# Kernel tuning notes

Measured on AMD Instinct MI355X. Metric: run time of the kernel, lower is better.

## Reference

```python
import jax, jax.numpy as jnp
import numpy as np

W_BITS = 8
A_BITS = 8


def sym_quant(x, num_bits):
    # Symmetric per-last-dim abs-max quantization (SymQuantizer.forward, ndim<=3,
    # layerwise=False): s = (2^(b-1)-1)/(max|x| + 1e-6); q = round(x*s)/(s+1e-6)
    max_abs = jnp.max(jnp.abs(x), axis=-1, keepdims=True)
    s = (2.0 ** (num_bits - 1) - 1.0) / (max_abs + 1e-6)
    return jnp.round(x * s) / (s + 1e-6)


def setup_inputs() -> dict:
    key = jax.random.key(0)
    kx, kw = jax.random.split(key)
    B, S, NX, NF = 4, 2048, 1600, 6400
    x = jax.random.normal(kx, (B, S, NX), dtype=jnp.float32)
    weight = 0.02 * jax.random.normal(kw, (NX, NF), dtype=jnp.float32)  # Conv1D: [nx, nf]
    bias = jnp.zeros((NF,), dtype=jnp.float32)
    return {"x": x, "weight": weight, "bias": bias}


def reference(x, weight, bias):
    # quantize weights per-row (over nf), quantize activations per-token (over nx)
    wq = sym_quant(weight, W_BITS)
    xq = sym_quant(x, A_BITS)
    # addmm(bias, x.view(-1, nx), weight) then reshape back
    return jnp.einsum("bsx,xf->bsf", xq, wq) + bias
```

## Files before the change

kernel.cpp:

```cpp
#include <hip/hip_runtime.h>
#include <stdint.h>

typedef _Float16 f16;
typedef _Float16 f16x4 __attribute__((ext_vector_type(4)));
typedef _Float16 f16x8 __attribute__((ext_vector_type(8)));
typedef float f32x4 __attribute__((ext_vector_type(4)));

#define K_DIM 1600
#define NF_DIM 6400
#define KPAD 1664
#define NKT 26
#define KPB (KPAD * 2)

#define ABYTES 32768
#define BBYTES 40960
#define BUFSZ (ABYTES + BBYTES)
#define BOFF ABYTES

__device__ __forceinline__ void async_copy16(const void* g, void* l) {
    __builtin_amdgcn_global_load_lds(
        (const __attribute__((address_space(1))) void*)(uintptr_t)g,
        (__attribute__((address_space(3))) void*)(uint32_t)(uintptr_t)l,
        16, 0, 0);
}

__device__ __forceinline__ float blockMax(float v, float* sm) {
#pragma unroll
    for (int off = 32; off > 0; off >>= 1)
        v = fmaxf(v, __shfl_down(v, off, 64));
    int wid = threadIdx.x >> 6, lane = threadIdx.x & 63;
    if (lane == 0) sm[wid] = v;
    __syncthreads();
    if (threadIdx.x == 0) {
        float m = sm[0];
        for (int i = 1; i < (int)(blockDim.x >> 6); ++i) m = fmaxf(m, sm[i]);
        sm[0] = m;
    }
    __syncthreads();
    return sm[0];
}

__global__ void quant_x_kernel(const float* __restrict__ x, f16* __restrict__ qx,
                               float* __restrict__ ax) {
    __shared__ float sm[4];
    size_t row = blockIdx.x;
    const float* xr = x + row * (size_t)K_DIM;
    float m = 0.f;
    const int n4 = K_DIM >> 2;
    for (int i = threadIdx.x; i < n4; i += blockDim.x) {
        float4 v = ((const float4*)xr)[i];
        m = fmaxf(fmaxf(fmaxf(fabsf(v.x), fabsf(v.y)), fmaxf(fabsf(v.z), fabsf(v.w))), m);
    }
    m = blockMax(m, sm);
    float s = 127.0f / (m + 1e-6f);
    if (threadIdx.x == 0) ax[row] = 1.0f / (s + 1e-6f);
    f16* qr = qx + row * (size_t)KPAD;
    for (int i = threadIdx.x; i < n4; i += blockDim.x) {
        float4 v = ((const float4*)xr)[i];
        f16x4 q;
        q[0] = (f16)rintf(v.x * s);
        q[1] = (f16)rintf(v.y * s);
        q[2] = (f16)rintf(v.z * s);
        q[3] = (f16)rintf(v.w * s);
        *(f16x4*)&qr[i * 4] = q;
    }
    if (threadIdx.x < 16) {
        f16x4 z = {};
        *(f16x4*)&qr[K_DIM + threadIdx.x * 4] = z;
    }
}

__global__ void wscale_kernel(const float* __restrict__ w, float* __restrict__ sw) {
    __shared__ float sm[4];
    size_t k = blockIdx.x;
    const float* wr = w + k * (size_t)NF_DIM;
    float m = 0.f;
    const int n4 = NF_DIM >> 2;
    for (int i = threadIdx.x; i < n4; i += blockDim.x) {
        float4 v = ((const float4*)wr)[i];
        m = fmaxf(fmaxf(fmaxf(fabsf(v.x), fabsf(v.y)), fmaxf(fabsf(v.z), fabsf(v.w))), m);
    }
    m = blockMax(m, sm);
    if (threadIdx.x == 0) sw[k] = 127.0f / (m + 1e-6f);
}

__global__ void wtq_kernel(const float* __restrict__ w, const float* __restrict__ sw,
                           f16* __restrict__ wqt) {
    __shared__ f16 t[64][80];
    int k0 = blockIdx.x * 64;
    int f0 = blockIdx.y * 64;
    int tid = threadIdx.x;
    if (k0 >= K_DIM) {
        int fr = tid >> 2;
        int ch = (tid & 3) << 4;
        float4 z = {};
        float4* dst = (float4*)&wqt[(size_t)(f0 + fr) * KPAD + k0 + ch];
        dst[0] = z;
        dst[1] = z;
        return;
    }
    int rr = tid >> 4;
    int cc = (tid & 15) << 2;
#pragma unroll
    for (int i = 0; i < 4; ++i) {
        int r = rr + i * 16;
        float s = sw[k0 + r];
        float inv = 1.0f / (s + 1e-6f);
        float4 v = *(const float4*)&w[(size_t)(k0 + r) * NF_DIM + f0 + cc];
        t[cc + 0][r] = (f16)(rintf(v.x * s) * inv);
        t[cc + 1][r] = (f16)(rintf(v.y * s) * inv);
        t[cc + 2][r] = (f16)(rintf(v.z * s) * inv);
        t[cc + 3][r] = (f16)(rintf(v.w * s) * inv);
    }
    __syncthreads();
    int fr = tid >> 2;
    int ch = (tid & 3) << 4;
    const float4* src = (const float4*)&t[fr][ch];
    float4* dst = (float4*)&wqt[(size_t)(f0 + fr) * KPAD + k0 + ch];
    dst[0] = src[0];
    dst[1] = src[1];
}

__global__ __launch_bounds__(512, 1) void gemm256x320(
    const f16* __restrict__ A,
    const f16* __restrict__ Bt,
    const float* __restrict__ ax,
    const float* __restrict__ bias,
    float* __restrict__ C, int M, int N) {
    extern __shared__ char lds[];

    const int tid = threadIdx.x;
    const int lane = tid & 63;
    const int wv = tid >> 6;
    const int wm = wv >> 2;
    const int wn = wv & 3;
    const int lr = lane & 15;
    const int lg = lane >> 4;

    const int bid = blockIdx.x;
    const int cpx = gridDim.x >> 3;
    const int swz = (bid & 7) * cpx + (bid >> 3);
    const int tm = swz & 31;
    const int tn = swz >> 5;
    const size_t m0 = (size_t)tm * 256, n0 = (size_t)tn * 320;

    const int srow8 = lane >> 3;
    const int sslot = (lane & 7) ^ srow8;
    const char* pA = (const char*)A + (m0 + (size_t)(wv * 32 + srow8)) * KPB + sslot * 16;
    const char* pB = (const char*)Bt + (n0 + (size_t)(wv * 40 + srow8)) * KPB + sslot * 16;
    const int LA0 = wv * 4096 + lane * 16;
    const int LB0 = BOFF + wv * 5120 + lane * 16;

#define ST_A(bufo, t)                                                          \
    {                                                                          \
        const char* g_ = pA + (size_t)(t) * 128;                               \
        _Pragma("unroll") for (int j_ = 0; j_ < 4; ++j_)                       \
            async_copy16(g_ + (size_t)(j_ * 8) * KPB,                          \
                         lds + (bufo) + LA0 + j_ * 1024);                      \
    }
#define ST_B(bufo, t)                                                          \
    {                                                                          \
        const char* g_ = pB + (size_t)(t) * 128;                               \
        _Pragma("unroll") for (int c_ = 0; c_ < 5; ++c_)                       \
            async_copy16(g_ + (size_t)(c_ * 8) * KPB,                          \
                         lds + (bufo) + LB0 + c_ * 1024);                      \
    }

    const int adr0 = (wm * 128 + lr) * 128 + ((((lg)) ^ (lr & 7)) << 4);
    const int adr1 = (wm * 128 + lr) * 128 + (((4 + lg) ^ (lr & 7)) << 4);
    const int bdr0 = BOFF + (wn * 80 + lr) * 128 + (((lg) ^ (lr & 7)) << 4);
    const int bdr1 = BOFF + (wn * 80 + lr) * 128 + (((4 + lg) ^ (lr & 7)) << 4);

#define RD_P(dst, bufo, p, AOFF)                                       \
    {                                                                  \
        const char* p_ = lds + (bufo) + (AOFF) + (p) * 4096;           \
        dst[0] = *(const f16x8*)(p_);                                  \
        dst[1] = *(const f16x8*)(p_ + 2048);                           \
    }
#define RD_B5(dst, bufo, BOFFK)                                        \
    {                                                                  \
        const char* p_ = lds + (bufo) + (BOFFK);                       \
        _Pragma("unroll") for (int n_ = 0; n_ < 5; ++n_)               \
            dst[n_] = *(const f16x8*)(p_ + n_ * 2048);                 \
    }
#define RD_B01(dst, bufo, BOFFK)                                       \
    {                                                                  \
        const char* p_ = lds + (bufo) + (BOFFK);                       \
        dst[0] = *(const f16x8*)(p_);                                  \
        dst[1] = *(const f16x8*)(p_ + 2048);                           \
    }
#define RD_B234(dst, bufo, BOFFK)                                      \
    {                                                                  \
        const char* p_ = lds + (bufo) + (BOFFK);                       \
        dst[2] = *(const f16x8*)(p_ + 2 * 2048);                       \
        dst[3] = *(const f16x8*)(p_ + 3 * 2048);                       \
        dst[4] = *(const f16x8*)(p_ + 4 * 2048);                       \
    }

#define BARRIER __builtin_amdgcn_s_barrier()
#define LGKM(n) asm volatile("s_waitcnt lgkmcnt(" #n ")" ::: "memory")
#define VM0 asm volatile("s_waitcnt vmcnt(0)" ::: "memory")
#define SB0 __builtin_amdgcn_sched_barrier(0)

#define MF10(AF, BF, R0)                                                          \
    {                                                                             \
        __builtin_amdgcn_s_setprio(1);                                            \
        _Pragma("unroll") for (int a_ = 0; a_ < 2; ++a_)                          \
        _Pragma("unroll") for (int n_ = 0; n_ < 5; ++n_)                          \
            acc[(R0) + a_][n_] = __builtin_amdgcn_mfma_f32_16x16x32_f16(          \
                AF[a_], BF[n_], acc[(R0) + a_][n_], 0, 0, 0);                     \
        __builtin_amdgcn_s_setprio(0);                                            \
    }

#define TILE(CUR, NXT, tn1)                                           \
    {                                                                 \
                                                             \
        RD_P(aN, CUR, 1, adr0);                                       \
        RD_B01(Bk1, CUR, bdr1);                                       \
        ST_A(NXT, tn1);                                               \
        LGKM(4); SB0;                                                 \
        MF10(aP, Bk0, 0);                                             \
                                                             \
        RD_P(aP, CUR, 2, adr0);                                       \
        RD_B234(Bk1, CUR, bdr1);                                      \
        LGKM(7); SB0;                                                 \
        MF10(aN, Bk0, 2);                                             \
                                                             \
        RD_P(aN, CUR, 3, adr0);                                       \
        ST_B(NXT, tn1);                                               \
        LGKM(5); SB0;                                                 \
        MF10(aP, Bk0, 4);                                             \
                                                             \
        RD_P(aP, CUR, 0, adr1);                                       \
        LGKM(2); SB0;                                                 \
        MF10(aN, Bk0, 6);                                             \
                                                             \
        RD_P(aN, CUR, 1, adr1);                                       \
        LGKM(2); SB0;                                                 \
        MF10(aP, Bk1, 0);                                             \
                                                             \
        RD_P(aP, CUR, 2, adr1);                                       \
        LGKM(2); SB0;                                                 \
        MF10(aN, Bk1, 2);                                             \
                                                             \
        RD_P(aN, CUR, 3, adr1);                                       \
        LGKM(2); SB0;                                                 \
        MF10(aP, Bk1, 4);                                             \
                                                             \
        VM0; LGKM(0); SB0;                                            \
        BARRIER;                                                      \
        RD_P(aP, NXT, 0, adr0);                                       \
        RD_B5(Bk0, NXT, bdr0);                                        \
        SB0;                                                          \
        MF10(aN, Bk1, 6);                                             \
    }

    f32x4 acc[8][5] = {};
    f16x8 aP[2], aN[2], Bk0[5], Bk1[5];

    ST_A(0, 0);
    ST_B(0, 0);
    VM0;
    BARRIER;
    RD_P(aP, 0, 0, adr0);
    RD_B5(Bk0, 0, bdr0);

    for (int i = 0; i < NKT / 2; ++i) {
        const int ta = 2 * i + 1;
        const int tb = (2 * i + 2 < NKT) ? 2 * i + 2 : NKT - 1;
        TILE(0, BUFSZ, ta);
        TILE(BUFSZ, 0, tb);
    }
    asm volatile("s_waitcnt vmcnt(0) lgkmcnt(0)" ::: "memory");

    float bv[5];
#pragma unroll
    for (int n_ = 0; n_ < 5; ++n_) bv[n_] = bias[n0 + wn * 80 + n_ * 16 + lr];
#pragma unroll
    for (int a = 0; a < 8; ++a) {
#pragma unroll
        for (int j = 0; j < 4; ++j) {
            size_t row = m0 + wm * 128 + a * 16 + lg * 4 + j;
            float axv = ax[row];
            float* crow = C + row * (size_t)N + n0 + wn * 80;
#pragma unroll
            for (int n_ = 0; n_ < 5; ++n_)
                crow[n_ * 16 + lr] = acc[a][n_][j] * axv + bv[n_];
        }
    }
}

extern "C" void kernel_launch(void* const* d_in, const int* in_sizes, int n_in,
                              void* d_out, int out_size, void* d_ws, size_t ws_size,
                              hipStream_t stream) {
    const float* x = (const float*)d_in[0];
    const float* w = (const float*)d_in[1];
    const float* bias = (const float*)d_in[2];
    float* out = (float*)d_out;

    const int M = in_sizes[0] / K_DIM;
    const int N = NF_DIM;

    char* ws = (char*)d_ws;
    f16* qx = (f16*)ws;
    f16* wqt = (f16*)(ws + (size_t)M * KPAD * 2);
    float* ax = (float*)(ws + (size_t)M * KPAD * 2 + (size_t)N * KPAD * 2);
    float* sw = ax + M;

    quant_x_kernel<<<M, 256, 0, stream>>>(x, qx, ax);
    wscale_kernel<<<K_DIM, 256, 0, stream>>>(w, sw);
    wtq_kernel<<<dim3(KPAD / 64, NF_DIM / 64), 256, 0, stream>>>(w, sw, wqt);

    (void)hipFuncSetAttribute((const void*)gemm256x320,
                              hipFuncAttributeMaxDynamicSharedMemorySize, 2 * BUFSZ);
    gemm256x320<<<(M / 256) * (N / 320), 512, 2 * BUFSZ, stream>>>(qx, wqt, ax, bias, out, M, N);
}
```

Measured before the change: 241.8 us.

## Shrink GEMM block tile to 128x320 with four waves per block

Cuts the GEMM workgroup from 8 waves on a 256x320 tile to 4 waves on a 128x320 tile, with each wave covering all 128 rows and an 80-column slice. The global-to-LDS copy mapping is redone for 256 threads, and B-tile loads are split into two batches spread across the pipeline. LDS per block roughly halves for A, and there are twice as many blocks for better CU fill and more concurrent blocks per CU. The cost is lower operand reuse per block, so total L2/HBM traffic for B goes up.

New measurement: 246.2 us. No clear change (+1.8%).

```diff
diff --git a/kernel.cpp b/kernel.cpp
--- a/kernel.cpp
+++ b/kernel.cpp
@@ -12,7 +12,7 @@
 #define NKT 26
 #define KPB (KPAD * 2)
 
-#define ABYTES 32768
+#define ABYTES 16384
 #define BBYTES 40960
 #define BUFSZ (ABYTES + BBYTES)
 #define BOFF ABYTES
@@ -121,7 +121,7 @@
     dst[1] = src[1];
 }
 
-__global__ __launch_bounds__(512, 1) void gemm256x320(
+__global__ __launch_bounds__(256, 1) void gemm128x320w4(
     const f16* __restrict__ A,
     const f16* __restrict__ Bt,
     const float* __restrict__ ax,
@@ -132,44 +132,41 @@
     const int tid = threadIdx.x;
     const int lane = tid & 63;
     const int wv = tid >> 6;
-    const int wm = wv >> 2;
-    const int wn = wv & 3;
     const int lr = lane & 15;
     const int lg = lane >> 4;
 
     const int bid = blockIdx.x;
     const int cpx = gridDim.x >> 3;
     const int swz = (bid & 7) * cpx + (bid >> 3);
-    const int tm = swz & 31;
-    const int tn = swz >> 5;
-    const size_t m0 = (size_t)tm * 256, n0 = (size_t)tn * 320;
-
-    const int srow8 = lane >> 3;
-    const int sslot = (lane & 7) ^ srow8;
-    const char* pA = (const char*)A + (m0 + (size_t)(wv * 32 + srow8)) * KPB + sslot * 16;
-    const char* pB = (const char*)Bt + (n0 + (size_t)(wv * 40 + srow8)) * KPB + sslot * 16;
-    const int LA0 = wv * 4096 + lane * 16;
-    const int LB0 = BOFF + wv * 5120 + lane * 16;
+    const int tm = swz & 63;
+    const int tn = swz >> 6;
+    const size_t m0 = (size_t)tm * 128, n0 = (size_t)tn * 320;
+
+    const int srow = tid >> 3;
+    const int sslot = (tid & 7) ^ (srow & 7);
+    const char* pA = (const char*)A + (m0 + (size_t)srow) * KPB + sslot * 16;
+    const char* pB = (const char*)Bt + (n0 + (size_t)srow) * KPB + sslot * 16;
+    const int LL0 = tid * 16;
 
 #define ST_A(bufo, t)                                                          \
     {                                                                          \
         const char* g_ = pA + (size_t)(t) * 128;                               \
         _Pragma("unroll") for (int j_ = 0; j_ < 4; ++j_)                       \
-            async_copy16(g_ + (size_t)(j_ * 8) * KPB,                          \
-                         lds + (bufo) + LA0 + j_ * 1024);                      \
-    }
-#define ST_B(bufo, t)                                                          \
+            async_copy16(g_ + (size_t)(j_ * 32) * KPB,                         \
+                         lds + (bufo) + LL0 + j_ * 4096);                      \
+    }
+#define ST_B5(bufo, t, c0)                                                     \
     {                                                                          \
         const char* g_ = pB + (size_t)(t) * 128;                               \
-        _Pragma("unroll") for (int c_ = 0; c_ < 5; ++c_)                       \
-            async_copy16(g_ + (size_t)(c_ * 8) * KPB,                          \
-                         lds + (bufo) + LB0 + c_ * 1024);                      \
-    }
-
-    const int adr0 = (wm * 128 + lr) * 128 + ((((lg)) ^ (lr & 7)) << 4);
-    const int adr1 = (wm * 128 + lr) * 128 + (((4 + lg) ^ (lr & 7)) << 4);
-    const int bdr0 = BOFF + (wn * 80 + lr) * 128 + (((lg) ^ (lr & 7)) << 4);
-    const int bdr1 = BOFF + (wn * 80 + lr) * 128 + (((4 + lg) ^ (lr & 7)) << 4);
+        _Pragma("unroll") for (int c_ = (c0); c_ < (c0) + 5; ++c_)             \
+            async_copy16(g_ + (size_t)(c_ * 32) * KPB,                         \
+                         lds + (bufo) + BOFF + LL0 + c_ * 4096);               \
+    }
+
+    const int adr0 = lr * 128 + (((lg) ^ (lr & 7)) << 4);
+    const int adr1 = lr * 128 + (((4 + lg) ^ (lr & 7)) << 4);
+    const int bdr0 = BOFF + (wv * 80 + lr) * 128 + (((lg) ^ (lr & 7)) << 4);
+    const int bdr1 = BOFF + (wv * 80 + lr) * 128 + (((4 + lg) ^ (lr & 7)) << 4);
 
 #define RD_P(dst, bufo, p, AOFF)                                       \
     {                                                                  \
@@ -223,11 +220,12 @@
                                                              \
         RD_P(aP, CUR, 2, adr0);                                       \
         RD_B234(Bk1, CUR, bdr1);                                      \
+        ST_B5(NXT, tn1, 0);                                           \
         LGKM(7); SB0;                                                 \
         MF10(aN, Bk0, 2);                                             \
                                                              \
         RD_P(aN, CUR, 3, adr0);                                       \
-        ST_B(NXT, tn1);                                               \
+        ST_B5(NXT, tn1, 5);                                           \
         LGKM(5); SB0;                                                 \
         MF10(aP, Bk0, 4);                                             \
                                                              \
@@ -259,7 +257,8 @@
     f16x8 aP[2], aN[2], Bk0[5], Bk1[5];
 
     ST_A(0, 0);
-    ST_B(0, 0);
+    ST_B5(0, 0, 0);
+    ST_B5(0, 0, 5);
     VM0;
     BARRIER;
     RD_P(aP, 0, 0, adr0);
@@ -275,14 +274,14 @@
 
     float bv[5];
 #pragma unroll
-    for (int n_ = 0; n_ < 5; ++n_) bv[n_] = bias[n0 + wn * 80 + n_ * 16 + lr];
+    for (int n_ = 0; n_ < 5; ++n_) bv[n_] = bias[n0 + wv * 80 + n_ * 16 + lr];
 #pragma unroll
     for (int a = 0; a < 8; ++a) {
 #pragma unroll
         for (int j = 0; j < 4; ++j) {
-            size_t row = m0 + wm * 128 + a * 16 + lg * 4 + j;
+            size_t row = m0 + a * 16 + lg * 4 + j;
             float axv = ax[row];
-            float* crow = C + row * (size_t)N + n0 + wn * 80;
+            float* crow = C + row * (size_t)N + n0 + wv * 80;
 #pragma unroll
             for (int n_ = 0; n_ < 5; ++n_)
                 crow[n_ * 16 + lr] = acc[a][n_][j] * axv + bv[n_];
@@ -311,7 +310,7 @@
     wscale_kernel<<<K_DIM, 256, 0, stream>>>(w, sw);
     wtq_kernel<<<dim3(KPAD / 64, NF_DIM / 64), 256, 0, stream>>>(w, sw, wqt);
 
-    (void)hipFuncSetAttribute((const void*)gemm256x320,
+    (void)hipFuncSetAttribute((const void*)gemm128x320w4,
                               hipFuncAttributeMaxDynamicSharedMemorySize, 2 * BUFSZ);
-    gemm256x320<<<(M / 256) * (N / 320), 512, 2 * BUFSZ, stream>>>(qx, wqt, ax, bias, out, M, N);
-}
+    gemm128x320w4<<<(M / 128) * (N / 320), 256, 2 * BUFSZ, stream>>>(qx, wqt, ax, bias, out, M, N);
+}
```
